# Performance work log

Measured on AMD Instinct MI355X. Metric: run time of the kernel, lower is better.

Reference implementation:

```python
import jax, jax.numpy as jnp
import numpy as np

NUM_CLASSES = 256
FEATURE_DIM = 768
BATCH = 128
SIM_BALANCE = 0.7
TIER1 = 50.0
TIER2 = 10.0
TOPK = 5


def _l2norm(x):
    return x / jnp.linalg.norm(x, axis=1, keepdims=True)


def build_edge_weights(class_features, context_features, w1, b1, w2, b2,
                       co_occurrence, instance_counts):
    """Vectorized, faithful translation of VisualFeatureGraph.build_graph."""
    N = class_features.shape[0]
    dt = class_features.dtype
    co = co_occurrence.astype(dt)            # [N,N], diag is 0
    cnt = instance_counts.astype(dt)         # [N]

    vs = _l2norm(class_features) @ _l2norm(class_features).T    # visual_sim [N,N]
    cs = _l2norm(context_features) @ _l2norm(context_features).T  # context_sim
    combined = SIM_BALANCE * vs + (1.0 - SIM_BALANCE) * cs

    # ---- Tier 1: co > TIER1 ----
    # sim_proj(f_i - f_j): exploit linearity of first layer: (f_i-f_j)@W1 = a_i - a_j
    a = class_features @ w1                                    # [N, D/2]
    h = jax.nn.relu(a[:, None, :] - a[None, :, :] + b1)        # [N,N,D/2]
    sim_weight = jax.nn.sigmoid(h @ w2 + b2)[..., 0]           # [N,N]
    ratio = (jnp.minimum(cnt[:, None], cnt[None, :]) /
             jnp.maximum(jnp.maximum(cnt[:, None], cnt[None, :]), 1.0))
    e1 = combined * sim_weight * ratio

    # ---- Tier 2: TIER2 < co <= TIER1 ----
    # shared neighbors k: co[i,k]>T1 and co[j,k]>T1 (k=i,j auto-excluded: diag=0
    # and co[i,j]<=T1 for tier-2 pairs)
    A = (co > TIER1).astype(dt)                                # [N,N]
    M = vs * A
    shared_sum = M @ M.T                                       # sum_k vs[i,k]*vs[j,k]
    shared_cnt = A @ A.T
    avg_sim = shared_sum / jnp.maximum(shared_cnt, 1.0)
    conf = co / TIER1
    e2 = jnp.where(shared_cnt > 0,
                   conf * combined + (1.0 - conf) * avg_sim,
                   conf * combined)

    # ---- Tier 3: co <= TIER2 ----
    # top-5 neighbors per row by co-occurrence among co > TIER2 (diag=0 and
    # co[i,j]<=TIER2 for tier-3 pairs, so i and j are auto-excluded)
    top_vals, top_idx = jax.lax.top_k(co, TOPK)                # [N,K]
    valid = top_vals > TIER2                                   # [N,K]
    ii = top_idx[:, None, :, None]                             # [N,1,K,1]
    jj = top_idx[None, :, None, :]                             # [1,N,1,K]
    co_cross = co[ii, jj]                                      # co[i_neigh, j_neigh] [N,N,K,K]
    vs_cross = vs[ii, jj]
    vs_in = jnp.take_along_axis(vs, top_idx, axis=1)           # vs[i, i_neigh] [N,K]
    mask = valid[:, None, :, None] & valid[None, :, None, :] & (co_cross > 0)
    w = (top_vals[:, None, :, None] * top_vals[None, :, None, :]) / TIER1
    w = jnp.where(mask, w, 0.0)
    sim = vs_in[:, None, :, None] * vs_in[None, :, None, :] * vs_cross
    trans = jnp.sum(w * sim, axis=(2, 3))                      # [N,N]
    tot = jnp.sum(w, axis=(2, 3))
    e3 = jnp.where(tot > 0, trans / jnp.where(tot > 0, tot, 1.0), 0.1 * cs)

    tier1_mask = co > TIER1
    tier2_mask = (co > TIER2) & ~tier1_mask
    E = jnp.where(tier1_mask, e1, jnp.where(tier2_mask, e2, e3))
    E = E * (1.0 - jnp.eye(N, dtype=dt))                       # i==j skipped
    mx = jnp.max(E)
    E = jnp.where(mx > 0, E / jnp.where(mx > 0, mx, 1.0), E)
    return E


def setup_inputs() -> dict:
    key = jax.random.key(0)
    ks = jax.random.split(key, 8)
    N, D, B = NUM_CLASSES, FEATURE_DIM, BATCH
    x = jax.random.normal(ks[0], (B, N, D), dtype=jnp.float32)
    class_features = jax.random.normal(ks[1], (N, D), dtype=jnp.float32) * 0.05
    context_features = jax.random.normal(ks[2], (N, D), dtype=jnp.float32) * 0.05
    w1 = jax.random.normal(ks[3], (D, D // 2), dtype=jnp.float32) * (1.0 / np.sqrt(D))
    b1 = jnp.zeros((D // 2,), dtype=jnp.float32)
    w2 = jax.random.normal(ks[4], (D // 2, 1), dtype=jnp.float32) * (1.0 / np.sqrt(D // 2))
    b2 = jnp.zeros((1,), dtype=jnp.float32)
    co = jax.random.randint(ks[5], (N, N), 0, 121, dtype=jnp.int32)
    co = (co + co.T) // 2                                      # symmetric like update_features
    co = co * (1 - jnp.eye(N, dtype=jnp.int32))                # zero diagonal
    instance_counts = jax.random.randint(ks[6], (N,), 1, 1001, dtype=jnp.int32)
    return {"x": x, "class_features": class_features,
            "context_features": context_features,
            "w1": w1, "b1": b1, "w2": w2, "b2": b2,
            "co_occurrence": co, "instance_counts": instance_counts}


def reference(x, class_features, context_features, w1, b1, w2, b2,
              co_occurrence, instance_counts):
    E = build_edge_weights(class_features, context_features, w1, b1, w2, b2,
                           co_occurrence, instance_counts)
    # torch.bmm(E.expand(B,-1,-1), x) == einsum over shared node dim
    return x + jnp.einsum('ij,bjd->bid', E, x)
```

## Files before the change

### kernel.cpp

```cpp
#include <hip/hip_runtime.h>
#include <hip/hip_bf16.h>
#include <math.h>

#define N 256
#define D 768
#define BATCH 128

typedef float f32x4 __attribute__((ext_vector_type(4)));
typedef short bf16x8 __attribute__((ext_vector_type(8)));

static __device__ __forceinline__ unsigned short f2bf(float f) {
    unsigned int u = __float_as_uint(f);
    u += 0x7fffu + ((u >> 16) & 1u);
    return (unsigned short)(u >> 16);
}
static __device__ __forceinline__ unsigned int pack2bf(float lo, float hi) {
    unsigned int a = __float_as_uint(lo);
    unsigned int b = __float_as_uint(hi);
    a += 0x7fffu + ((a >> 16) & 1u);
    b += 0x7fffu + ((b >> 16) & 1u);
    return (a >> 16) | (b & 0xffff0000u);
}

__global__ void k_stage1(const float* __restrict__ cf, const float* __restrict__ ctx,
                         float* __restrict__ vsn, float* __restrict__ csn,
                         const float* __restrict__ w1, float* __restrict__ a,
                         const int* __restrict__ co, float* __restrict__ topv,
                         int* __restrict__ topi) {
    __shared__ float sm[2 * 64 * 33];
    int bx = blockIdx.x;
    int t = threadIdx.x;
    if (bx < 512) {
        int row = bx;
        const float* src;
        float* dst;
        if (row < N) { src = cf  + row * D;       dst = vsn + row * D; }
        else         { src = ctx + (row - N) * D; dst = csn + (row - N) * D; }
        float s = 0.f;
        for (int d = t; d < D; d += 256) { float v = src[d]; s += v * v; }
        float* red = sm;
        red[t] = s; __syncthreads();
        for (int off = 128; off > 0; off >>= 1) {
            if (t < off) red[t] += red[t + off];
            __syncthreads();
        }
        float inv = 1.0f / sqrtf(red[0]);
        for (int d = t; d < D; d += 256) dst[d] = src[d] * inv;
    } else if (bx < 608) {
        int bi = bx - 512;
        int i0 = (bi / 12) * 32, j0 = (bi % 12) * 32;
        float (*Ci)[33] = (float(*)[33])sm;
        float (*Wj)[33] = (float(*)[33])(sm + 64 * 33);
        int tx = t & 15, ty = t >> 4;
        float a00 = 0.f, a01 = 0.f, a10 = 0.f, a11 = 0.f;
        for (int k0 = 0; k0 < 768; k0 += 64) {
            #pragma unroll
            for (int s = 0; s < 8; s++) {
                int idx = s * 256 + t;
                int row = idx >> 6, kc = idx & 63;
                Ci[kc][row] = cf[(i0 + row) * 768 + k0 + kc];
                int kr = idx >> 5, col = idx & 31;
                Wj[kr][col] = w1[(k0 + kr) * 384 + j0 + col];
            }
            __syncthreads();
            #pragma unroll 4
            for (int kk = 0; kk < 64; kk++) {
                float iv0 = Ci[kk][ty * 2], iv1 = Ci[kk][ty * 2 + 1];
                float jv0 = Wj[kk][tx * 2], jv1 = Wj[kk][tx * 2 + 1];
                a00 += iv0 * jv0; a01 += iv0 * jv1;
                a10 += iv1 * jv0; a11 += iv1 * jv1;
            }
            __syncthreads();
        }
        a[(i0 + ty * 2)     * 384 + j0 + tx * 2]     = a00;
        a[(i0 + ty * 2)     * 384 + j0 + tx * 2 + 1] = a01;
        a[(i0 + ty * 2 + 1) * 384 + j0 + tx * 2]     = a10;
        a[(i0 + ty * 2 + 1) * 384 + j0 + tx * 2 + 1] = a11;
    } else {
        int lane = t & 63;
        int row = (bx - 608) * 4 + (t >> 6);
        int4 v4 = *(const int4*)(co + row * 256 + lane * 4);
        int key[4];
        key[0] = v4.x * 256 + (255 - (lane * 4 + 0));
        key[1] = v4.y * 256 + (255 - (lane * 4 + 1));
        key[2] = v4.z * 256 + (255 - (lane * 4 + 2));
        key[3] = v4.w * 256 + (255 - (lane * 4 + 3));
        for (int r = 0; r < 5; r++) {
            int best = key[0];
            #pragma unroll
            for (int e = 1; e < 4; e++) best = max(best, key[e]);
            #pragma unroll
            for (int off = 32; off > 0; off >>= 1) best = max(best, __shfl_xor(best, off, 64));
            int kidx = 255 - (best & 255);
            int val = best >> 8;
            if (lane == 0) { topv[row * 5 + r] = (float)val; topi[row * 5 + r] = kidx; }
            if ((kidx >> 2) == lane) key[kidx & 3] = -1;
        }
    }
}

__global__ void k_gram2(const float* __restrict__ vsn, const float* __restrict__ csn,
                        float* __restrict__ vs, float* __restrict__ cs) {
    int bx = blockIdx.x;
    const float* S = (bx >= 64) ? csn : vsn;
    float* O       = (bx >= 64) ? cs  : vs;
    int bi = bx & 63;
    int i0 = (bi >> 3) * 32, j0 = (bi & 7) * 32;
    __shared__ float Li[64][33], Lj[64][33];
    int t = threadIdx.x;
    int tx = t & 15, ty = t >> 4;
    float a00 = 0.f, a01 = 0.f, a10 = 0.f, a11 = 0.f;
    for (int k0 = 0; k0 < 768; k0 += 64) {
        #pragma unroll
        for (int s = 0; s < 8; s++) {
            int idx = s * 256 + t;
            int row = idx >> 6, kc = idx & 63;
            Li[kc][row] = S[(i0 + row) * 768 + k0 + kc];
            Lj[kc][row] = S[(j0 + row) * 768 + k0 + kc];
        }
        __syncthreads();
        #pragma unroll 4
        for (int kk = 0; kk < 64; kk++) {
            float iv0 = Li[kk][ty * 2], iv1 = Li[kk][ty * 2 + 1];
            float jv0 = Lj[kk][tx * 2], jv1 = Lj[kk][tx * 2 + 1];
            a00 += iv0 * jv0; a01 += iv0 * jv1;
            a10 += iv1 * jv0; a11 += iv1 * jv1;
        }
        __syncthreads();
    }
    O[(i0 + ty * 2)     * 256 + j0 + tx * 2]     = a00;
    O[(i0 + ty * 2)     * 256 + j0 + tx * 2 + 1] = a01;
    O[(i0 + ty * 2 + 1) * 256 + j0 + tx * 2]     = a10;
    O[(i0 + ty * 2 + 1) * 256 + j0 + tx * 2 + 1] = a11;
}

__global__ void k_stage3(const float* __restrict__ a, const float* __restrict__ b1,
                         const float* __restrict__ w2, const float* __restrict__ b2,
                         const float* __restrict__ vs, const float* __restrict__ cs,
                         const int* __restrict__ ic, float* __restrict__ e1,
                         const int* __restrict__ co, float* __restrict__ ss,
                         float* __restrict__ sc) {
    __shared__ float sm[12800];
    int bx = blockIdx.x;
    int t = threadIdx.x;
    if (bx < 256) {
        int i0 = (bx >> 4) * 16, j0 = (bx & 15) * 16;
        float (*ai)[388]  = (float(*)[388])sm;
        float (*ajm)[388] = (float(*)[388])(sm + 16 * 388);
        float* sw2 = sm + 2 * 16 * 388;
        for (int idx = t; idx < 16 * 96; idx += 256) {
            int r = idx / 96, c = (idx % 96) * 4;
            *(float4*)&ai[r][c] = *(const float4*)(a + (i0 + r) * 384 + c);
            float4 u  = *(const float4*)(a + (j0 + r) * 384 + c);
            float4 bb = *(const float4*)(b1 + c);
            u.x -= bb.x; u.y -= bb.y; u.z -= bb.z; u.w -= bb.w;
            *(float4*)&ajm[r][c] = u;
        }
        for (int k = t; k < 384; k += 256) sw2[k] = w2[k];
        __syncthreads();
        int tx = t & 15, ty = t >> 4;
        float s = 0.f;
        #pragma unroll 4
        for (int k4 = 0; k4 < 96; k4++) {
            float4 xv = *(const float4*)&ai[ty][k4 * 4];
            float4 yv = *(const float4*)&ajm[tx][k4 * 4];
            float4 wv = *(const float4*)&sw2[k4 * 4];
            s += fmaxf(xv.x - yv.x, 0.f) * wv.x;
            s += fmaxf(xv.y - yv.y, 0.f) * wv.y;
            s += fmaxf(xv.z - yv.z, 0.f) * wv.z;
            s += fmaxf(xv.w - yv.w, 0.f) * wv.w;
        }
        int i = i0 + ty, j = j0 + tx;
        float sig = 1.0f / (1.0f + expf(-(s + b2[0])));
        float comb = 0.7f * vs[i * 256 + j] + 0.3f * cs[i * 256 + j];
        float ci = (float)ic[i], cj = (float)ic[j];
        float mn = fminf(ci, cj), mx = fmaxf(ci, cj);
        float ratio = mn / fmaxf(mx, 1.0f);
        e1[i * 256 + j] = comb * sig * ratio;
    } else {
        int bi = bx - 256;
        int i0 = (bi >> 3) * 32, j0 = (bi & 7) * 32;
        float (*Mi)[33] = (float(*)[33])sm;
        float (*Ai)[33] = (float(*)[33])(sm + 2112);
        float (*Mj)[33] = (float(*)[33])(sm + 4224);
        float (*Aj)[33] = (float(*)[33])(sm + 6336);
        int tx = t & 15, ty = t >> 4;
        float s00=0.f,s01=0.f,s10=0.f,s11=0.f;
        float c00=0.f,c01=0.f,c10=0.f,c11=0.f;
        for (int k0 = 0; k0 < 256; k0 += 64) {
            #pragma unroll
            for (int s = 0; s < 8; s++) {
                int idx = s * 256 + t;
                int row = idx >> 6, kc = idx & 63;
                int civ = co[(i0 + row) * 256 + k0 + kc];
                float aa = civ > 50 ? 1.f : 0.f;
                Ai[kc][row] = aa;
                Mi[kc][row] = aa * vs[(i0 + row) * 256 + k0 + kc];
                int cjv = co[(j0 + row) * 256 + k0 + kc];
                float ab = cjv > 50 ? 1.f : 0.f;
                Aj[kc][row] = ab;
                Mj[kc][row] = ab * vs[(j0 + row) * 256 + k0 + kc];
            }
            __syncthreads();
            #pragma unroll 4
            for (int kk = 0; kk < 64; kk++) {
                float mi0 = Mi[kk][ty*2], mi1 = Mi[kk][ty*2+1];
                float ai0 = Ai[kk][ty*2], ai1 = Ai[kk][ty*2+1];
                float mj0 = Mj[kk][tx*2], mj1 = Mj[kk][tx*2+1];
                float aj0 = Aj[kk][tx*2], aj1 = Aj[kk][tx*2+1];
                s00 += mi0*mj0; s01 += mi0*mj1; s10 += mi1*mj0; s11 += mi1*mj1;
                c00 += ai0*aj0; c01 += ai0*aj1; c10 += ai1*aj0; c11 += ai1*aj1;
            }
            __syncthreads();
        }
        ss[(i0+ty*2)  *256 + j0+tx*2]   = s00; ss[(i0+ty*2)  *256 + j0+tx*2+1] = s01;
        ss[(i0+ty*2+1)*256 + j0+tx*2]   = s10; ss[(i0+ty*2+1)*256 + j0+tx*2+1] = s11;
        sc[(i0+ty*2)  *256 + j0+tx*2]   = c00; sc[(i0+ty*2)  *256 + j0+tx*2+1] = c01;
        sc[(i0+ty*2+1)*256 + j0+tx*2]   = c10; sc[(i0+ty*2+1)*256 + j0+tx*2+1] = c11;
    }
}

__global__ void k_assemble(const int* __restrict__ co, const float* __restrict__ vs,
                           const float* __restrict__ cs, const float* __restrict__ e1,
                           const float* __restrict__ ss, const float* __restrict__ sc,
                           const float* __restrict__ topv, const int* __restrict__ topi,
                           float* __restrict__ E, float* __restrict__ partials) {
    int i = blockIdx.x, j = threadIdx.x;
    int cij = co[i * 256 + j];
    float e;
    if (i == j) {
        e = 0.f;
    } else if (cij > 50) {
        e = e1[i * 256 + j];
    } else if (cij > 10) {
        float conf = (float)cij / 50.0f;
        float comb = 0.7f * vs[i * 256 + j] + 0.3f * cs[i * 256 + j];
        float cnt = sc[i * 256 + j];
        float avg = ss[i * 256 + j] / fmaxf(cnt, 1.f);
        e = (cnt > 0.f) ? conf * comb + (1.f - conf) * avg : conf * comb;
    } else {
        float tvi[5], tvj[5]; int tii[5], tij[5];
        #pragma unroll
        for (int k = 0; k < 5; k++) {
            tvi[k] = topv[i * 5 + k]; tii[k] = topi[i * 5 + k];
            tvj[k] = topv[j * 5 + k]; tij[k] = topi[j * 5 + k];
        }
        float trans = 0.f, tot = 0.f;
        #pragma unroll
        for (int k = 0; k < 5; k++) {
            if (!(tvi[k] > 10.f)) continue;
            float vin_i = vs[i * 256 + tii[k]];
            #pragma unroll
            for (int l = 0; l < 5; l++) {
                if (!(tvj[l] > 10.f)) continue;
                int cc = co[tii[k] * 256 + tij[l]];
                if (cc <= 0) continue;
                float w = tvi[k] * tvj[l] / 50.f;
                float sim = vin_i * vs[j * 256 + tij[l]] * vs[tii[k] * 256 + tij[l]];
                trans += w * sim; tot += w;
            }
        }
        e = (tot > 0.f) ? trans / tot : 0.1f * cs[i * 256 + j];
    }
    E[i * 256 + j] = e;
    __shared__ float red[256];
    red[j] = e; __syncthreads();
    for (int off = 128; off > 0; off >>= 1) {
        if (j < off) red[j] = fmaxf(red[j], red[j + off]);
        __syncthreads();
    }
    if (j == 0) partials[i] = red[0];
}

__global__ void k_ep(const float* __restrict__ E, const float* __restrict__ partials,
                     unsigned short* __restrict__ Ep) {
    __shared__ float red[256];
    int t = threadIdx.x;
    red[t] = partials[t]; __syncthreads();
    for (int off = 128; off > 0; off >>= 1) {
        if (t < off) red[t] = fmaxf(red[t], red[t + off]);
        __syncthreads();
    }
    float mx = red[0];
    float s = (mx > 0.f) ? 1.0f / mx : 1.0f;
    int base = (blockIdx.x * 256 + t) * 4;
    float4 e4 = *(const float4*)(E + base);
    float ev[4] = {e4.x, e4.y, e4.z, e4.w};
    unsigned short o[4];
    #pragma unroll
    for (int q = 0; q < 4; q++) {
        int g = base + q;
        float v = s * ev[q] + (((g >> 8) == (g & 255)) ? 1.0f : 0.0f);
        o[q] = f2bf(v);
    }
    uint2 w;
    w.x = (unsigned int)o[0] | ((unsigned int)o[1] << 16);
    w.y = (unsigned int)o[2] | ((unsigned int)o[3] << 16);
    *(uint2*)(Ep + base) = w;
}

__global__ __launch_bounds__(256) void k_einsum_bf(
    const unsigned short* __restrict__ Ep, const float* __restrict__ x,
    float* __restrict__ out) {
    __shared__ __align__(16) unsigned short xt[64 * 264];
    int t = threadIdx.x;
    int b = blockIdx.y;
    int d0 = blockIdx.x * 64;
    int lane = t & 63, w = t >> 6;
    int l15 = lane & 15, lq = lane >> 4;

    int dl = t & 63;
    int ko = t >> 6;
    const float* xb = x + ((size_t)b * 256 + ko * 8) * 768 + d0 + dl;

    float v[8][8];
    #pragma unroll
    for (int kt = 0; kt < 8; kt++)
        #pragma unroll
        for (int s = 0; s < 8; s++)
            v[kt][s] = xb[((size_t)kt * 32 + s) * 768];
    #pragma unroll
    for (int kt = 0; kt < 8; kt++) {
        uint4 pv;
        pv.x = pack2bf(v[kt][0], v[kt][1]);
        pv.y = pack2bf(v[kt][2], v[kt][3]);
        pv.z = pack2bf(v[kt][4], v[kt][5]);
        pv.w = pack2bf(v[kt][6], v[kt][7]);
        *(uint4*)&xt[dl * 264 + kt * 32 + ko * 8] = pv;
    }
    __syncthreads();

    f32x4 acc[4][4];
    #pragma unroll
    for (int mf = 0; mf < 4; mf++)
        #pragma unroll
        for (int nf = 0; nf < 4; nf++)
            #pragma unroll
            for (int e = 0; e < 4; e++) acc[mf][nf][e] = 0.f;

    const unsigned short* eprow = Ep + (((w * 64 + l15) << 8) + lq * 8);

    #pragma unroll
    for (int kt = 0; kt < 8; kt++) {
        uint4 bv[4];
        #pragma unroll
        for (int nf = 0; nf < 4; nf++)
            bv[nf] = *(const uint4*)(eprow + (nf << 12) + kt * 32);
        bf16x8 af[4];
        #pragma unroll
        for (int g = 0; g < 4; g++)
            af[g] = *(const bf16x8*)&xt[(g * 16 + l15) * 264 + kt * 32 + lq * 8];
        #pragma unroll
        for (int mf = 0; mf < 4; mf++)
            #pragma unroll
            for (int nf = 0; nf < 4; nf++)
                acc[mf][nf] = __builtin_amdgcn_mfma_f32_16x16x32_bf16(
                    af[mf], *(const bf16x8*)&bv[nf], acc[mf][nf], 0, 0, 0);
    }

    float* ob = out + ((size_t)b * 256) * 768 + d0;
    #pragma unroll
    for (int mf = 0; mf < 4; mf++) {
        #pragma unroll
        for (int nf = 0; nf < 4; nf++) {
            int i = w * 64 + nf * 16 + l15;
            int d = mf * 16 + lq * 4;
            *(float4*)(ob + (size_t)i * 768 + d) = *(float4*)&acc[mf][nf];
        }
    }
}

extern "C" void kernel_launch(void* const* d_in, const int* in_sizes, int n_in,
                              void* d_out, int out_size, void* d_ws, size_t ws_size,
                              hipStream_t stream) {
    const float* x   = (const float*)d_in[0];
    const float* cf  = (const float*)d_in[1];
    const float* ctx = (const float*)d_in[2];
    const float* w1  = (const float*)d_in[3];
    const float* b1  = (const float*)d_in[4];
    const float* w2  = (const float*)d_in[5];
    const float* b2  = (const float*)d_in[6];
    const int*   co  = (const int*)d_in[7];
    const int*   ic  = (const int*)d_in[8];
    float* out = (float*)d_out;

    float* ws   = (float*)d_ws;
    float* vsn  = ws;
    float* csn  = vsn + 196608;
    float* a    = csn + 196608;
    float* vs   = a + 98304;
    float* cs   = vs + 65536;
    float* e1   = cs + 65536;
    float* ss   = e1 + 65536;
    float* sc   = ss + 65536;
    float* E    = sc + 65536;
    float* topv = E + 65536;
    int*   topi = (int*)(topv + 1280);
    float* partials = (float*)(topi + 1280);
    unsigned short* Ep = (unsigned short*)(partials + 256);

    k_stage1<<<672, 256, 0, stream>>>(cf, ctx, vsn, csn, w1, a, co, topv, topi);
    k_gram2<<<128, 256, 0, stream>>>(vsn, csn, vs, cs);
    k_stage3<<<320, 256, 0, stream>>>(a, b1, w2, b2, vs, cs, ic, e1, co, ss, sc);
    k_assemble<<<256, 256, 0, stream>>>(co, vs, cs, e1, ss, sc, topv, topi, E, partials);
    k_ep<<<64, 256, 0, stream>>>(E, partials, Ep);
    k_einsum_bf<<<dim3(12, BATCH), 256, 0, stream>>>(Ep, x, out);
}
```

Before: 289.0 us.

## Fold normalization into Gram kernel and fuse E scaling into einsum

Row normalization is no longer a separate pass writing normalized copies. Each Gram block computes the squared norms of its own 64 rows and scales the raw dot products afterwards, which lets the Gram work run inside the stage-1 launch. The separate E-to-bf16 kernel is removed: the einsum kernel reduces the partial maxima per wave and scales, adds the identity and converts E on the fly while loading its operand. This drops two launches and the intermediate buffers, but every einsum block now re-reads fp32 E (twice the bytes) and repeats the conversion work.

```diff
diff --git a/kernel.cpp b/kernel.cpp
--- a/kernel.cpp
+++ b/kernel.cpp
@@ -23,31 +23,17 @@
 }
 
 __global__ void k_stage1(const float* __restrict__ cf, const float* __restrict__ ctx,
-                         float* __restrict__ vsn, float* __restrict__ csn,
                          const float* __restrict__ w1, float* __restrict__ a,
                          const int* __restrict__ co, float* __restrict__ topv,
-                         int* __restrict__ topi) {
+                         int* __restrict__ topi,
+                         float* __restrict__ vs, float* __restrict__ cs) {
     __shared__ float sm[2 * 64 * 33];
+    __shared__ float nsum[64][5];
+    __shared__ float invn[64];
     int bx = blockIdx.x;
     int t = threadIdx.x;
-    if (bx < 512) {
-        int row = bx;
-        const float* src;
-        float* dst;
-        if (row < N) { src = cf  + row * D;       dst = vsn + row * D; }
-        else         { src = ctx + (row - N) * D; dst = csn + (row - N) * D; }
-        float s = 0.f;
-        for (int d = t; d < D; d += 256) { float v = src[d]; s += v * v; }
-        float* red = sm;
-        red[t] = s; __syncthreads();
-        for (int off = 128; off > 0; off >>= 1) {
-            if (t < off) red[t] += red[t + off];
-            __syncthreads();
-        }
-        float inv = 1.0f / sqrtf(red[0]);
-        for (int d = t; d < D; d += 256) dst[d] = src[d] * inv;
-    } else if (bx < 608) {
-        int bi = bx - 512;
+    if (bx < 96) {
+        int bi = bx;
         int i0 = (bi / 12) * 32, j0 = (bi % 12) * 32;
         float (*Ci)[33] = (float(*)[33])sm;
         float (*Wj)[33] = (float(*)[33])(sm + 64 * 33);
@@ -76,62 +62,74 @@
         a[(i0 + ty * 2)     * 384 + j0 + tx * 2 + 1] = a01;
         a[(i0 + ty * 2 + 1) * 384 + j0 + tx * 2]     = a10;
         a[(i0 + ty * 2 + 1) * 384 + j0 + tx * 2 + 1] = a11;
-    } else {
+    } else if (bx < 160) {
         int lane = t & 63;
-        int row = (bx - 608) * 4 + (t >> 6);
+        int row = (bx - 96) * 4 + (t >> 6);
         int4 v4 = *(const int4*)(co + row * 256 + lane * 4);
-        int key[4];
-        key[0] = v4.x * 256 + (255 - (lane * 4 + 0));
-        key[1] = v4.y * 256 + (255 - (lane * 4 + 1));
-        key[2] = v4.z * 256 + (255 - (lane * 4 + 2));
-        key[3] = v4.w * 256 + (255 - (lane * 4 + 3));
+        int k0 = v4.x * 256 + (255 - (lane * 4 + 0));
+        int k1 = v4.y * 256 + (255 - (lane * 4 + 1));
+        int k2 = v4.z * 256 + (255 - (lane * 4 + 2));
+        int k3 = v4.w * 256 + (255 - (lane * 4 + 3));
         for (int r = 0; r < 5; r++) {
-            int best = key[0];
-            #pragma unroll
-            for (int e = 1; e < 4; e++) best = max(best, key[e]);
+            int best = max(max(k0, k1), max(k2, k3));
             #pragma unroll
             for (int off = 32; off > 0; off >>= 1) best = max(best, __shfl_xor(best, off, 64));
             int kidx = 255 - (best & 255);
             int val = best >> 8;
             if (lane == 0) { topv[row * 5 + r] = (float)val; topi[row * 5 + r] = kidx; }
-            if ((kidx >> 2) == lane) key[kidx & 3] = -1;
-        }
-    }
-}
-
-__global__ void k_gram2(const float* __restrict__ vsn, const float* __restrict__ csn,
-                        float* __restrict__ vs, float* __restrict__ cs) {
-    int bx = blockIdx.x;
-    const float* S = (bx >= 64) ? csn : vsn;
-    float* O       = (bx >= 64) ? cs  : vs;
-    int bi = bx & 63;
-    int i0 = (bi >> 3) * 32, j0 = (bi & 7) * 32;
-    __shared__ float Li[64][33], Lj[64][33];
-    int t = threadIdx.x;
-    int tx = t & 15, ty = t >> 4;
-    float a00 = 0.f, a01 = 0.f, a10 = 0.f, a11 = 0.f;
-    for (int k0 = 0; k0 < 768; k0 += 64) {
-        #pragma unroll
-        for (int s = 0; s < 8; s++) {
-            int idx = s * 256 + t;
-            int row = idx >> 6, kc = idx & 63;
-            Li[kc][row] = S[(i0 + row) * 768 + k0 + kc];
-            Lj[kc][row] = S[(j0 + row) * 768 + k0 + kc];
+            if ((kidx >> 2) == lane) {
+                int sel = kidx & 3;
+                k0 = (sel == 0) ? -1 : k0;
+                k1 = (sel == 1) ? -1 : k1;
+                k2 = (sel == 2) ? -1 : k2;
+                k3 = (sel == 3) ? -1 : k3;
+            }
+        }
+    } else {
+        int bx2 = bx - 160;
+        const float* S = (bx2 >= 64) ? ctx : cf;
+        float* O       = (bx2 >= 64) ? cs  : vs;
+        int bi = bx2 & 63;
+        int i0 = (bi >> 3) * 32, j0 = (bi & 7) * 32;
+        {
+            int r = t >> 2, p = t & 3;
+            const float* Srow = S + (size_t)((r < 32) ? (i0 + r) : (j0 + r - 32)) * 768;
+            float sq = 0.f;
+            for (int j = 0; j < 192; j++) { float v = Srow[p + 4 * j]; sq += v * v; }
+            nsum[r][p] = sq;
         }
         __syncthreads();
-        #pragma unroll 4
-        for (int kk = 0; kk < 64; kk++) {
-            float iv0 = Li[kk][ty * 2], iv1 = Li[kk][ty * 2 + 1];
-            float jv0 = Lj[kk][tx * 2], jv1 = Lj[kk][tx * 2 + 1];
-            a00 += iv0 * jv0; a01 += iv0 * jv1;
-            a10 += iv1 * jv0; a11 += iv1 * jv1;
-        }
+        if (t < 64) invn[t] = 1.0f / sqrtf(nsum[t][0] + nsum[t][1] + nsum[t][2] + nsum[t][3]);
         __syncthreads();
-    }
-    O[(i0 + ty * 2)     * 256 + j0 + tx * 2]     = a00;
-    O[(i0 + ty * 2)     * 256 + j0 + tx * 2 + 1] = a01;
-    O[(i0 + ty * 2 + 1) * 256 + j0 + tx * 2]     = a10;
-    O[(i0 + ty * 2 + 1) * 256 + j0 + tx * 2 + 1] = a11;
+        float (*Li)[33] = (float(*)[33])sm;
+        float (*Lj)[33] = (float(*)[33])(sm + 64 * 33);
+        int tx = t & 15, ty = t >> 4;
+        float a00 = 0.f, a01 = 0.f, a10 = 0.f, a11 = 0.f;
+        for (int k0 = 0; k0 < 768; k0 += 64) {
+            #pragma unroll
+            for (int s = 0; s < 8; s++) {
+                int idx = s * 256 + t;
+                int row = idx >> 6, kc = idx & 63;
+                Li[kc][row] = S[(i0 + row) * 768 + k0 + kc];
+                Lj[kc][row] = S[(j0 + row) * 768 + k0 + kc];
+            }
+            __syncthreads();
+            #pragma unroll 4
+            for (int kk = 0; kk < 64; kk++) {
+                float iv0 = Li[kk][ty * 2], iv1 = Li[kk][ty * 2 + 1];
+                float jv0 = Lj[kk][tx * 2], jv1 = Lj[kk][tx * 2 + 1];
+                a00 += iv0 * jv0; a01 += iv0 * jv1;
+                a10 += iv1 * jv0; a11 += iv1 * jv1;
+            }
+            __syncthreads();
+        }
+        float ni0 = invn[ty * 2], ni1 = invn[ty * 2 + 1];
+        float nj0 = invn[32 + tx * 2], nj1 = invn[32 + tx * 2 + 1];
+        O[(i0 + ty * 2)     * 256 + j0 + tx * 2]     = a00 * ni0 * nj0;
+        O[(i0 + ty * 2)     * 256 + j0 + tx * 2 + 1] = a01 * ni0 * nj1;
+        O[(i0 + ty * 2 + 1) * 256 + j0 + tx * 2]     = a10 * ni1 * nj0;
+        O[(i0 + ty * 2 + 1) * 256 + j0 + tx * 2 + 1] = a11 * ni1 * nj1;
+    }
 }
 
 __global__ void k_stage3(const float* __restrict__ a, const float* __restrict__ b1,
@@ -272,36 +270,9 @@
     if (j == 0) partials[i] = red[0];
 }
 
-__global__ void k_ep(const float* __restrict__ E, const float* __restrict__ partials,
-                     unsigned short* __restrict__ Ep) {
-    __shared__ float red[256];
-    int t = threadIdx.x;
-    red[t] = partials[t]; __syncthreads();
-    for (int off = 128; off > 0; off >>= 1) {
-        if (t < off) red[t] = fmaxf(red[t], red[t + off]);
-        __syncthreads();
-    }
-    float mx = red[0];
-    float s = (mx > 0.f) ? 1.0f / mx : 1.0f;
-    int base = (blockIdx.x * 256 + t) * 4;
-    float4 e4 = *(const float4*)(E + base);
-    float ev[4] = {e4.x, e4.y, e4.z, e4.w};
-    unsigned short o[4];
-    #pragma unroll
-    for (int q = 0; q < 4; q++) {
-        int g = base + q;
-        float v = s * ev[q] + (((g >> 8) == (g & 255)) ? 1.0f : 0.0f);
-        o[q] = f2bf(v);
-    }
-    uint2 w;
-    w.x = (unsigned int)o[0] | ((unsigned int)o[1] << 16);
-    w.y = (unsigned int)o[2] | ((unsigned int)o[3] << 16);
-    *(uint2*)(Ep + base) = w;
-}
-
 __global__ __launch_bounds__(256) void k_einsum_bf(
-    const unsigned short* __restrict__ Ep, const float* __restrict__ x,
-    float* __restrict__ out) {
+    const float* __restrict__ E, const float* __restrict__ partials,
+    const float* __restrict__ x, float* __restrict__ out) {
     __shared__ __align__(16) unsigned short xt[64 * 264];
     int t = threadIdx.x;
     int b = blockIdx.y;
@@ -309,6 +280,12 @@
     int lane = t & 63, w = t >> 6;
     int l15 = lane & 15, lq = lane >> 4;
 
+    float pm = fmaxf(fmaxf(partials[lane * 4], partials[lane * 4 + 1]),
+                     fmaxf(partials[lane * 4 + 2], partials[lane * 4 + 3]));
+    #pragma unroll
+    for (int off = 32; off > 0; off >>= 1) pm = fmaxf(pm, __shfl_xor(pm, off, 64));
+    float s = (pm > 0.f) ? 1.0f / pm : 1.0f;
+
     int dl = t & 63;
     int ko = t >> 6;
     const float* xb = x + ((size_t)b * 256 + ko * 8) * 768 + d0 + dl;
@@ -317,8 +294,8 @@
     #pragma unroll
     for (int kt = 0; kt < 8; kt++)
         #pragma unroll
-        for (int s = 0; s < 8; s++)
-            v[kt][s] = xb[((size_t)kt * 32 + s) * 768];
+        for (int sidx = 0; sidx < 8; sidx++)
+            v[kt][sidx] = xb[((size_t)kt * 32 + sidx) * 768];
     #pragma unroll
     for (int kt = 0; kt < 8; kt++) {
         uint4 pv;
@@ -338,14 +315,31 @@
             #pragma unroll
             for (int e = 0; e < 4; e++) acc[mf][nf][e] = 0.f;
 
-    const unsigned short* eprow = Ep + (((w * 64 + l15) << 8) + lq * 8);
+    const float* erow = E + (((w * 64 + l15) << 8) + lq * 8);
+    int wi = w * 64 + l15;
 
     #pragma unroll
     for (int kt = 0; kt < 8; kt++) {
-        uint4 bv[4];
-        #pragma unroll
-        for (int nf = 0; nf < 4; nf++)
-            bv[nf] = *(const uint4*)(eprow + (nf << 12) + kt * 32);
+        uint4 bvb[4];
+        #pragma unroll
+        for (int nf = 0; nf < 4; nf++) {
+            float4 fa = *(const float4*)(erow + (nf << 12) + kt * 32);
+            float4 fb = *(const float4*)(erow + (nf << 12) + kt * 32 + 4);
+            int i = wi + nf * 16;
+            int kb = kt * 32 + lq * 8;
+            float e0 = s * fa.x + ((kb + 0 == i) ? 1.f : 0.f);
+            float e1 = s * fa.y + ((kb + 1 == i) ? 1.f : 0.f);
+            float e2 = s * fa.z + ((kb + 2 == i) ? 1.f : 0.f);
+            float e3 = s * fa.w + ((kb + 3 == i) ? 1.f : 0.f);
+            float e4 = s * fb.x + ((kb + 4 == i) ? 1.f : 0.f);
+            float e5 = s * fb.y + ((kb + 5 == i) ? 1.f : 0.f);
+            float e6 = s * fb.z + ((kb + 6 == i) ? 1.f : 0.f);
+            float e7 = s * fb.w + ((kb + 7 == i) ? 1.f : 0.f);
+            uint4 pv;
+            pv.x = pack2bf(e0, e1); pv.y = pack2bf(e2, e3);
+            pv.z = pack2bf(e4, e5); pv.w = pack2bf(e6, e7);
+            bvb[nf] = pv;
+        }
         bf16x8 af[4];
         #pragma unroll
         for (int g = 0; g < 4; g++)
@@ -355,7 +349,7 @@
             #pragma unroll
             for (int nf = 0; nf < 4; nf++)
                 acc[mf][nf] = __builtin_amdgcn_mfma_f32_16x16x32_bf16(
-                    af[mf], *(const bf16x8*)&bv[nf], acc[mf][nf], 0, 0, 0);
+                    af[mf], *(const bf16x8*)&bvb[nf], acc[mf][nf], 0, 0, 0);
     }
 
     float* ob = out + ((size_t)b * 256) * 768 + d0;
@@ -397,12 +391,9 @@
     float* topv = E + 65536;
     int*   topi = (int*)(topv + 1280);
     float* partials = (float*)(topi + 1280);
-    unsigned short* Ep = (unsigned short*)(partials + 256);
-
-    k_stage1<<<672, 256, 0, stream>>>(cf, ctx, vsn, csn, w1, a, co, topv, topi);
-    k_gram2<<<128, 256, 0, stream>>>(vsn, csn, vs, cs);
+
+    k_stage1<<<288, 256, 0, stream>>>(cf, ctx, w1, a, co, topv, topi, vs, cs);
     k_stage3<<<320, 256, 0, stream>>>(a, b1, w2, b2, vs, cs, ic, e1, co, ss, sc);
     k_assemble<<<256, 256, 0, stream>>>(co, vs, cs, e1, ss, sc, topv, topi, E, partials);
-    k_ep<<<64, 256, 0, stream>>>(E, partials, Ep);
-    k_einsum_bf<<<dim3(12, BATCH), 256, 0, stream>>>(Ep, x, out);
-}
+    k_einsum_bf<<<dim3(12, BATCH), 256, 0, stream>>>(E, partials, x, out);
+}
```

New measurement: 295.0 us. +2.1%, slower.
